# Kernel optimization log

Measured on AMD Instinct MI355X. Metric: run time of the kernel, lower is better.

## Reference

```python
import jax, jax.numpy as jnp
import numpy as np

D_MODEL = 1024
N_HEADS = 16
D_K = D_MODEL // N_HEADS  # 64
THETA = 10000.0
MAX_SEQ_LEN = 2048
GPT_INIT_STD = 0.02


def _apply_rope(x, token_positions):
    """x: (b, h, t, d_k); token_positions: (b_or_1, t) int.
    Even/odd interleaved rotation, matching the torch RoPE module."""
    d_half = D_K // 2
    j = jnp.arange(d_half, dtype=jnp.float32)
    inv_freq = THETA ** (-2.0 * j / float(D_K))              # (d_half,)
    angles = token_positions.astype(jnp.float32)[..., None] * inv_freq  # (b, t, d_half)
    cos = jnp.cos(angles)[:, None, :, :].astype(x.dtype)     # (b, 1, t, d_half)
    sin = jnp.sin(angles)[:, None, :, :].astype(x.dtype)
    x_even = x[..., 0::2]
    x_odd = x[..., 1::2]
    r_even = x_even * cos - x_odd * sin
    r_odd = x_even * sin + x_odd * cos
    return jnp.stack([r_even, r_odd], axis=-1).reshape(x.shape)


def setup_inputs() -> dict:
    key = jax.random.key(0)
    kx, kq, kk, kv, ko = jax.random.split(key, 5)
    B, T = 2, 2048
    x = jax.random.normal(kx, (B, T, D_MODEL), dtype=jnp.float32)
    # torch nn.Linear stores weight as (out_features, in_features); y = x @ W.T
    Wq = (jax.random.normal(kq, (D_MODEL, D_MODEL), dtype=jnp.float32) * GPT_INIT_STD)
    Wk = (jax.random.normal(kk, (D_MODEL, D_MODEL), dtype=jnp.float32) * GPT_INIT_STD)
    Wv = (jax.random.normal(kv, (D_MODEL, D_MODEL), dtype=jnp.float32) * GPT_INIT_STD)
    Wo = (jax.random.normal(ko, (D_MODEL, D_MODEL), dtype=jnp.float32) * GPT_INIT_STD)
    token_positions = jnp.arange(T, dtype=jnp.int32)[None, :]  # (1, T), monotonic
    return {"x": x, "Wq": Wq, "Wk": Wk, "Wv": Wv, "Wo": Wo,
            "token_positions": token_positions}


def reference(x, Wq, Wk, Wv, Wo, token_positions):
    B, T, _ = x.shape
    # QKV projections (bias-free linear, torch convention y = x @ W.T)
    Q = (x @ Wq.T).reshape(B, T, N_HEADS, D_K).transpose(0, 2, 1, 3)  # (b,h,t,d)
    K = (x @ Wk.T).reshape(B, T, N_HEADS, D_K).transpose(0, 2, 1, 3)
    V = (x @ Wv.T).reshape(B, T, N_HEADS, D_K).transpose(0, 2, 1, 3)

    Q = _apply_rope(Q, token_positions)
    K = _apply_rope(K, token_positions)

    scaling = 1.0 / np.sqrt(D_K).astype(np.float32)
    scores = jnp.einsum('bhqd,bhkd->bhqk', Q, K) * scaling    # (b,h,t,t)
    # causal mask: key position <= query position (positions are monotonic)
    qp = token_positions  # (1 or b, t)
    causal = qp[:, None, :] <= qp[:, :, None]                 # (b_or_1, t, t)
    causal = causal[:, None, :, :]                            # (b_or_1, 1, t, t)
    neg = jnp.finfo(scores.dtype).min
    scores = jnp.where(causal, scores, neg)
    attn = jax.nn.softmax(scores.astype(jnp.float32), axis=-1).astype(x.dtype)
    out = jnp.einsum('bhqk,bhkd->bhqd', attn, V)              # (b,h,t,d)
    out = out.transpose(0, 2, 1, 3).reshape(B, T, D_MODEL)
    return out @ Wo.T
```

## Files before the change

kernel.cpp:

```cpp
#include <hip/hip_runtime.h>
#include <hip/hip_bf16.h>

typedef __attribute__((ext_vector_type(8))) __bf16 bf16x8;
typedef __attribute__((ext_vector_type(4))) float f32x4;

#define T_SEQ   2048
#define DMODEL  1024

__device__ __forceinline__ void gload_lds16(const void* g, void* l) {
  __builtin_amdgcn_global_load_lds((const __attribute__((address_space(1))) void*)g,
                                   (__attribute__((address_space(3))) void*)l, 16, 0, 0);
}
#define VMCNT0() asm volatile("s_waitcnt vmcnt(0)" ::: "memory")

__global__ __launch_bounds__(256) void f32_to_bf16_k(const float* __restrict__ s,
                                                     __bf16* __restrict__ d, int n) {
  int i = (blockIdx.x * 256 + threadIdx.x) * 8;
  if (i >= n) return;
  float4 a = *(const float4*)(s + i);
  float4 b = *(const float4*)(s + i + 4);
  bf16x8 o;
  o[0] = (__bf16)a.x; o[1] = (__bf16)a.y; o[2] = (__bf16)a.z; o[3] = (__bf16)a.w;
  o[4] = (__bf16)b.x; o[5] = (__bf16)b.y; o[6] = (__bf16)b.z; o[7] = (__bf16)b.w;
  *(bf16x8*)(d + i) = o;
}

__global__ __launch_bounds__(256) void rope_table_k(const int* __restrict__ pos,
                                                    float2* __restrict__ tbl) {
  int idx = blockIdx.x * 256 + threadIdx.x;
  int t = idx >> 5, j = idx & 31;
  float p = (float)pos[t];
  float inv = powf(10000.0f, -(float)j * (1.0f / 32.0f));
  float a = p * inv;
  tbl[idx] = make_float2(cosf(a), sinf(a));
}

template <typename OutT>
__global__ __launch_bounds__(256) void gemm_bt(const __bf16* __restrict__ A,
                                               const __bf16* __restrict__ W,
                                               OutT* __restrict__ C,
                                               int M, int N, int K) {
  __shared__ alignas(16) __bf16 At[128 * 32];
  __shared__ alignas(16) __bf16 Bt[128 * 32];
  const int tid = threadIdx.x, w = tid >> 6, l = tid & 63;
  const int l16 = l & 15, lq = l >> 4;
  const int wm = w >> 1, wn = w & 1;
  const int br = blockIdx.y * 128, bc = blockIdx.x * 128;
  f32x4 acc[4][4] = {};
  const int off = w * 1024 + l * 16;
  const int rA = off >> 6, cA = off & 63;

  for (int kt = 0; kt < K; kt += 32) {
    __syncthreads();
    gload_lds16((const char*)A + ((size_t)(br + rA) * K + kt) * 2 + cA,
                (char*)At + w * 1024);
    gload_lds16((const char*)A + ((size_t)(br + 64 + rA) * K + kt) * 2 + cA,
                (char*)At + 4096 + w * 1024);
    gload_lds16((const char*)W + ((size_t)(bc + rA) * K + kt) * 2 + cA,
                (char*)Bt + w * 1024);
    gload_lds16((const char*)W + ((size_t)(bc + 64 + rA) * K + kt) * 2 + cA,
                (char*)Bt + 4096 + w * 1024);
    __syncthreads();

    bf16x8 af[4], bfr[4];
#pragma unroll
    for (int m = 0; m < 4; ++m)
      af[m] = *(const bf16x8*)(At + (wm * 64 + m * 16 + l16) * 32 + lq * 8);
#pragma unroll
    for (int n = 0; n < 4; ++n)
      bfr[n] = *(const bf16x8*)(Bt + (wn * 64 + n * 16 + l16) * 32 + lq * 8);
#pragma unroll
    for (int m = 0; m < 4; ++m)
#pragma unroll
      for (int n = 0; n < 4; ++n)
        acc[m][n] = __builtin_amdgcn_mfma_f32_16x16x32_bf16(af[m], bfr[n], acc[m][n], 0, 0, 0);
  }

#pragma unroll
  for (int m = 0; m < 4; ++m)
#pragma unroll
    for (int n = 0; n < 4; ++n)
#pragma unroll
      for (int r = 0; r < 4; ++r) {
        int row = br + wm * 64 + m * 16 + lq * 4 + r;
        int col = bc + wn * 64 + n * 16 + l16;
        float v = acc[m][n][r];
        if constexpr (__is_same(OutT, float))
          C[(size_t)row * N + col] = v;
        else
          C[(size_t)row * N + col] = (__bf16)v;
      }
}

__global__ __launch_bounds__(256) void gemm_qkv_k(const __bf16* __restrict__ A,
                                                  const __bf16* __restrict__ W,
                                                  __bf16* __restrict__ qr,
                                                  __bf16* __restrict__ kr,
                                                  __bf16* __restrict__ vt,
                                                  const float2* __restrict__ tbl) {
  __shared__ alignas(16) __bf16 At[128 * 32];
  __shared__ alignas(16) __bf16 Bt[128 * 32];
  const int K = 1024;
  const int tid = threadIdx.x, w = tid >> 6, l = tid & 63;
  const int l16 = l & 15, lq = l >> 4;
  const int wm = w >> 1, wn = w & 1;
  const int br = blockIdx.y * 128, bc = blockIdx.x * 128;
  f32x4 acc[4][4] = {};
  const int off = w * 1024 + l * 16;
  const int rA = off >> 6, cA = off & 63;

  for (int kt = 0; kt < K; kt += 32) {
    __syncthreads();
    gload_lds16((const char*)A + ((size_t)(br + rA) * K + kt) * 2 + cA,
                (char*)At + w * 1024);
    gload_lds16((const char*)A + ((size_t)(br + 64 + rA) * K + kt) * 2 + cA,
                (char*)At + 4096 + w * 1024);
    gload_lds16((const char*)W + ((size_t)(bc + rA) * K + kt) * 2 + cA,
                (char*)Bt + w * 1024);
    gload_lds16((const char*)W + ((size_t)(bc + 64 + rA) * K + kt) * 2 + cA,
                (char*)Bt + 4096 + w * 1024);
    __syncthreads();

    bf16x8 af[4], bfr[4];
#pragma unroll
    for (int m = 0; m < 4; ++m)
      af[m] = *(const bf16x8*)(At + (wm * 64 + m * 16 + l16) * 32 + lq * 8);
#pragma unroll
    for (int n = 0; n < 4; ++n)
      bfr[n] = *(const bf16x8*)(Bt + (wn * 64 + n * 16 + l16) * 32 + lq * 8);
#pragma unroll
    for (int m = 0; m < 4; ++m)
#pragma unroll
      for (int n = 0; n < 4; ++n)
        acc[m][n] = __builtin_amdgcn_mfma_f32_16x16x32_bf16(af[m], bfr[n], acc[m][n], 0, 0, 0);
  }

  const int sec = bc >> 10;
  const int cb = bc & 1023;
  if (sec == 2) {
#pragma unroll
    for (int m = 0; m < 4; ++m)
#pragma unroll
      for (int n = 0; n < 4; ++n)
#pragma unroll
        for (int r = 0; r < 4; ++r) {
          int row = br + wm * 64 + m * 16 + lq * 4 + r;
          int col = cb + wn * 64 + n * 16 + l16;
          int b = row >> 11, t = row & 2047, h = col >> 6, d = col & 63;
          vt[((size_t)((b * 16 + h) * 64 + d)) * T_SEQ + t] = (__bf16)acc[m][n][r];
        }
  } else {
    __bf16* dst = (sec == 0) ? qr : kr;
#pragma unroll
    for (int m = 0; m < 4; ++m)
#pragma unroll
      for (int n = 0; n < 4; ++n)
#pragma unroll
        for (int r = 0; r < 4; ++r) {
          float v = acc[m][n][r];
          float p = __shfl_xor(v, 1);
          int row = br + wm * 64 + m * 16 + lq * 4 + r;
          int col = cb + wn * 64 + n * 16 + l16;
          int b = row >> 11, t = row & 2047, h = col >> 6, d = col & 63;
          float2 cs = tbl[t * 32 + (d >> 1)];
          float o = v * cs.x + ((d & 1) ? p * cs.y : -(p * cs.y));
          dst[((size_t)((b * 16 + h) * T_SEQ + t)) * 64 + d] = (__bf16)o;
        }
  }
}

__global__ __launch_bounds__(256) void attn_k(const __bf16* __restrict__ Qr,
                                              const __bf16* __restrict__ Kr,
                                              const __bf16* __restrict__ Vt,
                                              __bf16* __restrict__ out) {
  __shared__ alignas(16) __bf16 Kt[2][64 * 64];
  __shared__ alignas(16) __bf16 Vtl[2][64 * 64];
  __shared__ alignas(16) __bf16 Pt[4][16 * 64];
  const int bh = blockIdx.x, qb0 = blockIdx.y * 64;
  const int tid = threadIdx.x, w = tid >> 6, l = tid & 63;
  const int l16 = l & 15, lq = l >> 4;

  const __bf16* Qbase = Qr + ((size_t)bh * T_SEQ + qb0 + w * 16) * 64;
  bf16x8 aq0 = *(const bf16x8*)(Qbase + l16 * 64 + lq * 8);
  bf16x8 aq1 = *(const bf16x8*)(Qbase + l16 * 64 + 32 + lq * 8);

  float mrow[4], lrow[4]; f32x4 acc[4] = {};
#pragma unroll
  for (int r = 0; r < 4; ++r) { mrow[r] = -1e30f; lrow[r] = 0.0f; }

  const int nt = qb0 / 64 + 1;
  const int offbase = w * 1024 + l * 16;

  auto stage = [&](int bufi, int kt) {
#pragma unroll
    for (int c2 = 0; c2 < 2; ++c2) {
      int o = offbase + c2 * 4096;
      int row = o >> 7, cbyte = o & 127;
      int sw = cbyte ^ ((row & 7) << 4);
      gload_lds16((const char*)Kr + ((size_t)(bh * T_SEQ + kt + row) * 64) * 2 + sw,
                  (char*)(&Kt[bufi][0]) + w * 1024 + c2 * 4096);
      gload_lds16((const char*)Vt + ((size_t)(bh * 64 + row) * T_SEQ + kt) * 2 + sw,
                  (char*)(&Vtl[bufi][0]) + w * 1024 + c2 * 4096);
    }
  };

  stage(0, 0);
  VMCNT0();
  __builtin_amdgcn_s_barrier();

  int buf = 0;
  for (int t = 0; t < nt; ++t) {
    const int kt = t * 64;
    if (t + 1 < nt) stage(buf ^ 1, kt + 64);

    const char* K0 = (const char*)&Kt[buf][0];
    const char* V0 = (const char*)&Vtl[buf][0];

    f32x4 s[4] = {};
#pragma unroll
    for (int g = 0; g < 4; ++g) {
      int row = g * 16 + l16;
      int x = (row & 7) << 4;
      bf16x8 b0 = *(const bf16x8*)(K0 + row * 128 + ((lq * 16) ^ x));
      s[g] = __builtin_amdgcn_mfma_f32_16x16x32_bf16(aq0, b0, s[g], 0, 0, 0);
      bf16x8 b1 = *(const bf16x8*)(K0 + row * 128 + ((lq * 16 + 64) ^ x));
      s[g] = __builtin_amdgcn_mfma_f32_16x16x32_bf16(aq1, b1, s[g], 0, 0, 0);
    }

    const bool diag = (t == nt - 1);
    const int qrow_base = qb0 + w * 16;
#pragma unroll
    for (int r = 0; r < 4; ++r) {
      int q = qrow_base + lq * 4 + r;
      float v0 = s[0][r] * 0.125f, v1 = s[1][r] * 0.125f;
      float v2 = s[2][r] * 0.125f, v3 = s[3][r] * 0.125f;
      if (diag) {
        if (kt + l16 > q)      v0 = -1e30f;
        if (kt + 16 + l16 > q) v1 = -1e30f;
        if (kt + 32 + l16 > q) v2 = -1e30f;
        if (kt + 48 + l16 > q) v3 = -1e30f;
      }
      float m = fmaxf(fmaxf(v0, v1), fmaxf(v2, v3));
      m = fmaxf(m, __shfl_xor(m, 1));
      m = fmaxf(m, __shfl_xor(m, 2));
      m = fmaxf(m, __shfl_xor(m, 4));
      m = fmaxf(m, __shfl_xor(m, 8));
      float mn = fmaxf(mrow[r], m);
      float alpha = __expf(mrow[r] - mn);
      float p0 = __expf(v0 - mn), p1 = __expf(v1 - mn);
      float p2 = __expf(v2 - mn), p3 = __expf(v3 - mn);
      float rs = (p0 + p1) + (p2 + p3);
      rs += __shfl_xor(rs, 1);
      rs += __shfl_xor(rs, 2);
      rs += __shfl_xor(rs, 4);
      rs += __shfl_xor(rs, 8);
      lrow[r] = lrow[r] * alpha + rs;
      mrow[r] = mn;
#pragma unroll
      for (int dt = 0; dt < 4; ++dt) acc[dt][r] *= alpha;
      int prow = lq * 4 + r;
      int px = (prow & 7) << 4;
      char* Pw = (char*)&Pt[w][0] + prow * 128;
      *(__bf16*)(Pw + ((l16 * 2) ^ px))      = (__bf16)p0;
      *(__bf16*)(Pw + ((32 + l16 * 2) ^ px)) = (__bf16)p1;
      *(__bf16*)(Pw + ((64 + l16 * 2) ^ px)) = (__bf16)p2;
      *(__bf16*)(Pw + ((96 + l16 * 2) ^ px)) = (__bf16)p3;
    }

#pragma unroll
    for (int ks = 0; ks < 2; ++ks) {
      bf16x8 ap = *(const bf16x8*)((const char*)&Pt[w][0] + l16 * 128 +
                                   ((ks * 64 + lq * 16) ^ ((l16 & 7) << 4)));
#pragma unroll
      for (int dt = 0; dt < 4; ++dt) {
        int row = dt * 16 + l16;
        bf16x8 bv = *(const bf16x8*)(V0 + row * 128 +
                                     ((ks * 64 + lq * 16) ^ ((row & 7) << 4)));
        acc[dt] = __builtin_amdgcn_mfma_f32_16x16x32_bf16(ap, bv, acc[dt], 0, 0, 0);
      }
    }

    VMCNT0();
    __builtin_amdgcn_s_barrier();
    buf ^= 1;
  }

  const int b = bh >> 4, h = bh & 15;
#pragma unroll
  for (int r = 0; r < 4; ++r) {
    float inv = 1.0f / lrow[r];
    size_t row = (size_t)b * T_SEQ + qb0 + w * 16 + lq * 4 + r;
#pragma unroll
    for (int dt = 0; dt < 4; ++dt)
      out[row * DMODEL + h * 64 + dt * 16 + l16] = (__bf16)(acc[dt][r] * inv);
  }
}

extern "C" void kernel_launch(void* const* d_in, const int* in_sizes, int n_in,
                              void* d_out, int out_size, void* d_ws, size_t ws_size,
                              hipStream_t stream) {
  const float* x  = (const float*)d_in[0];
  const float* Wq = (const float*)d_in[1];
  const float* Wk = (const float*)d_in[2];
  const float* Wv = (const float*)d_in[3];
  const float* Wo = (const float*)d_in[4];
  const int* pos  = (const int*)d_in[5];

  char* ws = (char*)d_ws;
  __bf16* xb   = (__bf16*)(ws + 0);
  __bf16* wqkv = (__bf16*)(ws + (8u << 20));
  __bf16* wob  = (__bf16*)(ws + (14u << 20));
  __bf16* qr   = (__bf16*)(ws + (16u << 20));
  __bf16* kr   = (__bf16*)(ws + (24u << 20));
  __bf16* vt   = (__bf16*)(ws + (32u << 20));
  __bf16* ao   = (__bf16*)(ws + (40u << 20));
  float2* tbl  = (float2*)(ws + (48u << 20));

  f32_to_bf16_k<<<2048, 256, 0, stream>>>(x, xb, 4194304);
  f32_to_bf16_k<<<512, 256, 0, stream>>>(Wq, wqkv, 1048576);
  f32_to_bf16_k<<<512, 256, 0, stream>>>(Wk, wqkv + 1048576, 1048576);
  f32_to_bf16_k<<<512, 256, 0, stream>>>(Wv, wqkv + 2097152, 1048576);
  f32_to_bf16_k<<<512, 256, 0, stream>>>(Wo, wob, 1048576);

  rope_table_k<<<256, 256, 0, stream>>>(pos, tbl);

  gemm_qkv_k<<<dim3(24, 32), 256, 0, stream>>>(xb, wqkv, qr, kr, vt, tbl);

  attn_k<<<dim3(32, 32), 256, 0, stream>>>(qr, kr, vt, ao);

  gemm_bt<float><<<dim3(8, 32), 256, 0, stream>>>(ao, wob, (float*)d_out, 4096, DMODEL, DMODEL);
}
```

Measured before the change: 251.4 us.

## Transpose MFMA operands, lazy softmax rescale, vectorized stores, fuse weight casts

Swaps the A/B operands of the MFMAs in the QKV GEMM and attention so each lane holds four consecutive columns. This enables packed bf16x4 stores for Q/K (with RoPE applied on register pairs and the 1/sqrt(d) scale folded into Q), for P in LDS, and for the attention output. The softmax now keeps one row per lane and skips the accumulator rescale unless the max grows by more than a threshold. The four weight conversion launches are merged into one kernel, and s_setprio hints are added around the MFMA blocks. Together these cut shuffles, scalar stores and launch overhead, at the cost of a lazy-max scheme that depends on fp32 headroom.

```diff
diff --git a/kernel.cpp b/kernel.cpp
--- a/kernel.cpp
+++ b/kernel.cpp
@@ -2,6 +2,7 @@
 #include <hip/hip_bf16.h>
 
 typedef __attribute__((ext_vector_type(8))) __bf16 bf16x8;
+typedef __attribute__((ext_vector_type(4))) __bf16 bf16x4;
 typedef __attribute__((ext_vector_type(4))) float f32x4;
 
 #define T_SEQ   2048
@@ -23,6 +24,24 @@
   o[0] = (__bf16)a.x; o[1] = (__bf16)a.y; o[2] = (__bf16)a.z; o[3] = (__bf16)a.w;
   o[4] = (__bf16)b.x; o[5] = (__bf16)b.y; o[6] = (__bf16)b.z; o[7] = (__bf16)b.w;
   *(bf16x8*)(d + i) = o;
+}
+
+__global__ __launch_bounds__(256) void w_to_bf16_k(const float* __restrict__ Wq,
+                                                   const float* __restrict__ Wk,
+                                                   const float* __restrict__ Wv,
+                                                   const float* __restrict__ Wo,
+                                                   __bf16* __restrict__ wqkv,
+                                                   __bf16* __restrict__ wob) {
+  int i = (blockIdx.x * 256 + threadIdx.x) * 8;
+  int sec = i >> 20, o = i & 1048575;
+  const float* s = (sec == 0) ? Wq : (sec == 1) ? Wk : (sec == 2) ? Wv : Wo;
+  __bf16* d = (sec == 3) ? (wob + o) : (wqkv + i);
+  float4 a = *(const float4*)(s + o);
+  float4 b = *(const float4*)(s + o + 4);
+  bf16x8 v;
+  v[0] = (__bf16)a.x; v[1] = (__bf16)a.y; v[2] = (__bf16)a.z; v[3] = (__bf16)a.w;
+  v[4] = (__bf16)b.x; v[5] = (__bf16)b.y; v[6] = (__bf16)b.z; v[7] = (__bf16)b.w;
+  *(bf16x8*)d = v;
 }
 
 __global__ __launch_bounds__(256) void rope_table_k(const int* __restrict__ pos,
@@ -129,43 +148,49 @@
     for (int n = 0; n < 4; ++n)
       bfr[n] = *(const bf16x8*)(Bt + (wn * 64 + n * 16 + l16) * 32 + lq * 8);
 #pragma unroll
-    for (int m = 0; m < 4; ++m)
-#pragma unroll
-      for (int n = 0; n < 4; ++n)
-        acc[m][n] = __builtin_amdgcn_mfma_f32_16x16x32_bf16(af[m], bfr[n], acc[m][n], 0, 0, 0);
+    for (int n = 0; n < 4; ++n)
+#pragma unroll
+      for (int m = 0; m < 4; ++m)
+        acc[n][m] = __builtin_amdgcn_mfma_f32_16x16x32_bf16(bfr[n], af[m], acc[n][m], 0, 0, 0);
   }
 
   const int sec = bc >> 10;
   const int cb = bc & 1023;
   if (sec == 2) {
 #pragma unroll
-    for (int m = 0; m < 4; ++m)
-#pragma unroll
-      for (int n = 0; n < 4; ++n)
-#pragma unroll
-        for (int r = 0; r < 4; ++r) {
-          int row = br + wm * 64 + m * 16 + lq * 4 + r;
-          int col = cb + wn * 64 + n * 16 + l16;
-          int b = row >> 11, t = row & 2047, h = col >> 6, d = col & 63;
-          vt[((size_t)((b * 16 + h) * 64 + d)) * T_SEQ + t] = (__bf16)acc[m][n][r];
-        }
+    for (int n = 0; n < 4; ++n)
+#pragma unroll
+      for (int m = 0; m < 4; ++m) {
+        int d0 = cb + wn * 64 + n * 16 + lq * 4;
+        int h = d0 >> 6, dk = d0 & 63;
+        int t = br + wm * 64 + m * 16 + l16;
+        int b = t >> 11, tt = t & 2047;
+#pragma unroll
+        for (int r = 0; r < 4; ++r)
+          vt[((size_t)((b * 16 + h) * 64 + dk + r)) * T_SEQ + tt] = (__bf16)acc[n][m][r];
+      }
   } else {
     __bf16* dst = (sec == 0) ? qr : kr;
-#pragma unroll
-    for (int m = 0; m < 4; ++m)
-#pragma unroll
-      for (int n = 0; n < 4; ++n)
-#pragma unroll
-        for (int r = 0; r < 4; ++r) {
-          float v = acc[m][n][r];
-          float p = __shfl_xor(v, 1);
-          int row = br + wm * 64 + m * 16 + lq * 4 + r;
-          int col = cb + wn * 64 + n * 16 + l16;
-          int b = row >> 11, t = row & 2047, h = col >> 6, d = col & 63;
-          float2 cs = tbl[t * 32 + (d >> 1)];
-          float o = v * cs.x + ((d & 1) ? p * cs.y : -(p * cs.y));
-          dst[((size_t)((b * 16 + h) * T_SEQ + t)) * 64 + d] = (__bf16)o;
-        }
+    const float sc = (sec == 0) ? 0.125f : 1.0f;
+#pragma unroll
+    for (int n = 0; n < 4; ++n)
+#pragma unroll
+      for (int m = 0; m < 4; ++m) {
+        int d0 = cb + wn * 64 + n * 16 + lq * 4;
+        int h = d0 >> 6, dk = d0 & 63;
+        int t = br + wm * 64 + m * 16 + l16;
+        int b = t >> 11, tt = t & 2047;
+        float2 cs0 = tbl[tt * 32 + (dk >> 1)];
+        float2 cs1 = tbl[tt * 32 + (dk >> 1) + 1];
+        float v0 = acc[n][m][0], v1 = acc[n][m][1];
+        float v2 = acc[n][m][2], v3 = acc[n][m][3];
+        bf16x4 pk;
+        pk[0] = (__bf16)((v0 * cs0.x - v1 * cs0.y) * sc);
+        pk[1] = (__bf16)((v0 * cs0.y + v1 * cs0.x) * sc);
+        pk[2] = (__bf16)((v2 * cs1.x - v3 * cs1.y) * sc);
+        pk[3] = (__bf16)((v2 * cs1.y + v3 * cs1.x) * sc);
+        *(bf16x4*)(dst + ((size_t)((b * 16 + h) * T_SEQ + tt)) * 64 + dk) = pk;
+      }
   }
 }
 
@@ -179,14 +204,14 @@
   const int bh = blockIdx.x, qb0 = blockIdx.y * 64;
   const int tid = threadIdx.x, w = tid >> 6, l = tid & 63;
   const int l16 = l & 15, lq = l >> 4;
+  const int px = (l16 & 7) << 4;
 
   const __bf16* Qbase = Qr + ((size_t)bh * T_SEQ + qb0 + w * 16) * 64;
   bf16x8 aq0 = *(const bf16x8*)(Qbase + l16 * 64 + lq * 8);
   bf16x8 aq1 = *(const bf16x8*)(Qbase + l16 * 64 + 32 + lq * 8);
 
-  float mrow[4], lrow[4]; f32x4 acc[4] = {};
-#pragma unroll
-  for (int r = 0; r < 4; ++r) { mrow[r] = -1e30f; lrow[r] = 0.0f; }
+  float mrow = -1e30f, lrow = 0.0f;
+  f32x4 acc[4] = {};
 
   const int nt = qb0 / 64 + 1;
   const int offbase = w * 1024 + l * 16;
@@ -217,68 +242,77 @@
     const char* V0 = (const char*)&Vtl[buf][0];
 
     f32x4 s[4] = {};
+    __builtin_amdgcn_s_setprio(1);
 #pragma unroll
     for (int g = 0; g < 4; ++g) {
       int row = g * 16 + l16;
       int x = (row & 7) << 4;
-      bf16x8 b0 = *(const bf16x8*)(K0 + row * 128 + ((lq * 16) ^ x));
-      s[g] = __builtin_amdgcn_mfma_f32_16x16x32_bf16(aq0, b0, s[g], 0, 0, 0);
-      bf16x8 b1 = *(const bf16x8*)(K0 + row * 128 + ((lq * 16 + 64) ^ x));
-      s[g] = __builtin_amdgcn_mfma_f32_16x16x32_bf16(aq1, b1, s[g], 0, 0, 0);
-    }
-
-    const bool diag = (t == nt - 1);
-    const int qrow_base = qb0 + w * 16;
-#pragma unroll
-    for (int r = 0; r < 4; ++r) {
-      int q = qrow_base + lq * 4 + r;
-      float v0 = s[0][r] * 0.125f, v1 = s[1][r] * 0.125f;
-      float v2 = s[2][r] * 0.125f, v3 = s[3][r] * 0.125f;
-      if (diag) {
-        if (kt + l16 > q)      v0 = -1e30f;
-        if (kt + 16 + l16 > q) v1 = -1e30f;
-        if (kt + 32 + l16 > q) v2 = -1e30f;
-        if (kt + 48 + l16 > q) v3 = -1e30f;
-      }
-      float m = fmaxf(fmaxf(v0, v1), fmaxf(v2, v3));
-      m = fmaxf(m, __shfl_xor(m, 1));
-      m = fmaxf(m, __shfl_xor(m, 2));
-      m = fmaxf(m, __shfl_xor(m, 4));
-      m = fmaxf(m, __shfl_xor(m, 8));
-      float mn = fmaxf(mrow[r], m);
-      float alpha = __expf(mrow[r] - mn);
-      float p0 = __expf(v0 - mn), p1 = __expf(v1 - mn);
-      float p2 = __expf(v2 - mn), p3 = __expf(v3 - mn);
-      float rs = (p0 + p1) + (p2 + p3);
-      rs += __shfl_xor(rs, 1);
-      rs += __shfl_xor(rs, 2);
-      rs += __shfl_xor(rs, 4);
-      rs += __shfl_xor(rs, 8);
-      lrow[r] = lrow[r] * alpha + rs;
-      mrow[r] = mn;
-#pragma unroll
-      for (int dt = 0; dt < 4; ++dt) acc[dt][r] *= alpha;
-      int prow = lq * 4 + r;
-      int px = (prow & 7) << 4;
-      char* Pw = (char*)&Pt[w][0] + prow * 128;
-      *(__bf16*)(Pw + ((l16 * 2) ^ px))      = (__bf16)p0;
-      *(__bf16*)(Pw + ((32 + l16 * 2) ^ px)) = (__bf16)p1;
-      *(__bf16*)(Pw + ((64 + l16 * 2) ^ px)) = (__bf16)p2;
-      *(__bf16*)(Pw + ((96 + l16 * 2) ^ px)) = (__bf16)p3;
-    }
-
+      bf16x8 k0 = *(const bf16x8*)(K0 + row * 128 + ((lq * 16) ^ x));
+      s[g] = __builtin_amdgcn_mfma_f32_16x16x32_bf16(k0, aq0, s[g], 0, 0, 0);
+      bf16x8 k1 = *(const bf16x8*)(K0 + row * 128 + ((lq * 16 + 64) ^ x));
+      s[g] = __builtin_amdgcn_mfma_f32_16x16x32_bf16(k1, aq1, s[g], 0, 0, 0);
+    }
+    __builtin_amdgcn_s_setprio(0);
+
+    if (t == nt - 1) {
+      int q = qb0 + w * 16 + l16;
+#pragma unroll
+      for (int g = 0; g < 4; ++g)
+#pragma unroll
+        for (int r = 0; r < 4; ++r)
+          if (kt + g * 16 + lq * 4 + r > q) s[g][r] = -1e30f;
+    }
+
+    float pm = -1e30f;
+#pragma unroll
+    for (int g = 0; g < 4; ++g)
+#pragma unroll
+      for (int r = 0; r < 4; ++r) pm = fmaxf(pm, s[g][r]);
+    pm = fmaxf(pm, __shfl_xor(pm, 16));
+    pm = fmaxf(pm, __shfl_xor(pm, 32));
+
+    if (__any(pm > mrow + 8.0f)) {
+      float mn = fmaxf(mrow, pm);
+      float alpha = __expf(mrow - mn);
+#pragma unroll
+      for (int dt = 0; dt < 4; ++dt)
+#pragma unroll
+        for (int r = 0; r < 4; ++r) acc[dt][r] *= alpha;
+      lrow *= alpha;
+      mrow = mn;
+    }
+
+    char* Pw = (char*)&Pt[w][0] + l16 * 128;
+    float rs = 0.0f;
+#pragma unroll
+    for (int g = 0; g < 4; ++g) {
+      bf16x4 pk;
+#pragma unroll
+      for (int r = 0; r < 4; ++r) {
+        float p = __expf(s[g][r] - mrow);
+        rs += p;
+        pk[r] = (__bf16)p;
+      }
+      *(bf16x4*)(Pw + ((g * 32 + lq * 8) ^ px)) = pk;
+    }
+    rs += __shfl_xor(rs, 16);
+    rs += __shfl_xor(rs, 32);
+    lrow += rs;
+
+    __builtin_amdgcn_s_setprio(1);
 #pragma unroll
     for (int ks = 0; ks < 2; ++ks) {
       bf16x8 ap = *(const bf16x8*)((const char*)&Pt[w][0] + l16 * 128 +
-                                   ((ks * 64 + lq * 16) ^ ((l16 & 7) << 4)));
+                                   ((ks * 64 + lq * 16) ^ px));
 #pragma unroll
       for (int dt = 0; dt < 4; ++dt) {
-        int row = dt * 16 + l16;
-        bf16x8 bv = *(const bf16x8*)(V0 + row * 128 +
-                                     ((ks * 64 + lq * 16) ^ ((row & 7) << 4)));
-        acc[dt] = __builtin_amdgcn_mfma_f32_16x16x32_bf16(ap, bv, acc[dt], 0, 0, 0);
-      }
-    }
+        int vrow = dt * 16 + l16;
+        bf16x8 vf = *(const bf16x8*)(V0 + vrow * 128 +
+                                     ((ks * 64 + lq * 16) ^ ((vrow & 7) << 4)));
+        acc[dt] = __builtin_amdgcn_mfma_f32_16x16x32_bf16(vf, ap, acc[dt], 0, 0, 0);
+      }
+    }
+    __builtin_amdgcn_s_setprio(0);
 
     VMCNT0();
     __builtin_amdgcn_s_barrier();
@@ -286,13 +320,14 @@
   }
 
   const int b = bh >> 4, h = bh & 15;
-#pragma unroll
-  for (int r = 0; r < 4; ++r) {
-    float inv = 1.0f / lrow[r];
-    size_t row = (size_t)b * T_SEQ + qb0 + w * 16 + lq * 4 + r;
-#pragma unroll
-    for (int dt = 0; dt < 4; ++dt)
-      out[row * DMODEL + h * 64 + dt * 16 + l16] = (__bf16)(acc[dt][r] * inv);
+  float inv = 1.0f / lrow;
+  size_t row = (size_t)b * T_SEQ + qb0 + w * 16 + l16;
+#pragma unroll
+  for (int dt = 0; dt < 4; ++dt) {
+    bf16x4 o;
+#pragma unroll
+    for (int r = 0; r < 4; ++r) o[r] = (__bf16)(acc[dt][r] * inv);
+    *(bf16x4*)(out + row * DMODEL + h * 64 + dt * 16 + lq * 4) = o;
   }
 }
 
@@ -317,11 +352,7 @@
   float2* tbl  = (float2*)(ws + (48u << 20));
 
   f32_to_bf16_k<<<2048, 256, 0, stream>>>(x, xb, 4194304);
-  f32_to_bf16_k<<<512, 256, 0, stream>>>(Wq, wqkv, 1048576);
-  f32_to_bf16_k<<<512, 256, 0, stream>>>(Wk, wqkv + 1048576, 1048576);
-  f32_to_bf16_k<<<512, 256, 0, stream>>>(Wv, wqkv + 2097152, 1048576);
-  f32_to_bf16_k<<<512, 256, 0, stream>>>(Wo, wob, 1048576);
-
+  w_to_bf16_k<<<2048, 256, 0, stream>>>(Wq, Wk, Wv, Wo, wqkv, wob);
   rope_table_k<<<256, 256, 0, stream>>>(pos, tbl);
 
   gemm_qkv_k<<<dim3(24, 32), 256, 0, stream>>>(xb, wqkv, qr, kr, vt, tbl);
```

After: 218.3 us. 13.2% less time.
